# Optimization experiments

Hardware: AMD Instinct MI355X
Metric: run time of the kernel (lower is better)

## Reference

```python
import jax, jax.numpy as jnp
import numpy as np

B, S, D = 2, 2048, 1024
H = 16
DH = D // H  # 64

def setup_inputs() -> dict:
    key = jax.random.key(0)
    k1, k2, k3, k4 = jax.random.split(key, 4)
    scale = 0.02
    x = jax.random.normal(k1, (B, S, D), dtype=jnp.float32)
    W_query = jax.random.normal(k2, (D, D), dtype=jnp.float32) * scale
    W_key = jax.random.normal(k3, (D, D), dtype=jnp.float32) * scale
    W_value = jax.random.normal(k4, (D, D), dtype=jnp.float32) * scale
    return {"x": x, "W_query": W_query, "W_key": W_key, "W_value": W_value}

def reference(x, W_query, W_key, W_value):
    b, n, d_in = x.shape
    # project and split heads: [b, h, n, dh]
    q = (x @ W_query).reshape(b, n, H, DH).transpose(0, 2, 1, 3)
    k = (x @ W_key).reshape(b, n, H, DH).transpose(0, 2, 1, 3)
    v = (x @ W_value).reshape(b, n, H, DH).transpose(0, 2, 1, 3)
    # raw scores, then causal mask (strict upper triangle -> -inf)
    scores = jnp.einsum('bhqd,bhkd->bhqk', q, k)
    causal = jnp.tril(jnp.ones((n, n), dtype=bool))  # True = keep
    scores = jnp.where(causal, scores, -jnp.inf)
    weights = jax.nn.softmax(scores / jnp.sqrt(jnp.float32(DH)), axis=-1)
    ctx = jnp.einsum('bhqk,bhkd->bhqd', weights, v)
    return ctx.transpose(0, 2, 1, 3).reshape(b, n, H * DH)
```

## Files before the change

### kernel.cpp

```cpp
#include <hip/hip_runtime.h>
#include <hip/hip_bf16.h>

#define S_LEN   2048
#define D_MODEL 1024
#define N_HEADS 16
#define D_HEAD  64
#define HEAD_ELEMS (2048ull * 64ull)
#define MAT_ELEMS  (4096ull * 1024ull)
#define W_ELEMS    (1024ull * 1024ull)

typedef __attribute__((ext_vector_type(8))) short short8_t;
typedef __attribute__((ext_vector_type(4))) short short4_t;
typedef __attribute__((ext_vector_type(4))) float f32x4;

__device__ __forceinline__ short f2bf(float f) {
    __hip_bfloat16 h = __float2bfloat16(f);
    union { __hip_bfloat16 h; short s; } cv;
    cv.h = h;
    return cv.s;
}

#define GLD_LDS16(gptr, lptr) \
    __builtin_amdgcn_global_load_lds( \
        (const __attribute__((address_space(1))) unsigned int*)(gptr), \
        (__attribute__((address_space(3))) unsigned int*)(lptr), 16, 0, 0)

__global__ __launch_bounds__(256) void convert_x_kernel(
    const float* __restrict__ x, short* __restrict__ xb)
{
    const int i = (blockIdx.x * 256 + threadIdx.x) * 8;
    const float4 v0 = *(const float4*)(x + i);
    const float4 v1 = *(const float4*)(x + i + 4);
    short8_t u;
    u[0] = f2bf(v0.x); u[1] = f2bf(v0.y); u[2] = f2bf(v0.z); u[3] = f2bf(v0.w);
    u[4] = f2bf(v1.x); u[5] = f2bf(v1.y); u[6] = f2bf(v1.z); u[7] = f2bf(v1.w);
    *(short8_t*)(xb + i) = u;
}

__global__ __launch_bounds__(256) void transpose_w_kernel(
    const float* __restrict__ Wq, const float* __restrict__ Wk,
    const float* __restrict__ Wv, short* __restrict__ wt)
{
    const int k0 = blockIdx.x * 64;
    const int n0 = blockIdx.y * 64;
    const int which = blockIdx.z;
    const float* W = (which == 0) ? Wq : (which == 1) ? Wk : Wv;
    short* out = wt + (size_t)which * W_ELEMS;

    __shared__ float Ts[64][68];
    const int t = threadIdx.x;
    {
        const int c4 = (t & 15) * 4;
#pragma unroll
        for (int i = 0; i < 4; ++i) {
            const int r = (t >> 4) + i * 16;
            const float4 v = *(const float4*)(W + (size_t)(k0 + r) * D_MODEL + n0 + c4);
            Ts[c4 + 0][r] = v.x; Ts[c4 + 1][r] = v.y;
            Ts[c4 + 2][r] = v.z; Ts[c4 + 3][r] = v.w;
        }
    }
    __syncthreads();
    const int nl = t >> 2;
#pragma unroll
    for (int s = 0; s < 2; ++s) {
        const int koff = (t & 3) * 8 + s * 32;
        short8_t u;
#pragma unroll
        for (int j = 0; j < 8; ++j) u[j] = f2bf(Ts[nl][koff + j]);
        *(short8_t*)(out + (size_t)(n0 + nl) * D_MODEL + k0 + koff) = u;
    }
}

__global__ __launch_bounds__(256, 3) void qkv_mfma_gemm_kernel(
    const short* __restrict__ xb,
    const short* __restrict__ wt,
    short* __restrict__ qkv)
{
    const int mBlock = blockIdx.x * 128;
    const int nBlock = blockIdx.y * 128;
    const int which  = blockIdx.z;
    const short* Bt = wt + (size_t)which * W_ELEMS;
    short* outBase  = qkv + (size_t)which * MAT_ELEMS;

    __shared__ short As[128 * 32];
    __shared__ short Bs[128 * 32];

    const int t    = threadIdx.x;
    const int w    = t >> 6;
    const int lane = t & 63;
    const int n16  = lane & 15;
    const int quad = lane >> 4;
    const int mq   = (w & 1) * 64;
    const int nq   = (w >> 1) * 64;

    f32x4 acc[4][4];
#pragma unroll
    for (int i = 0; i < 4; ++i)
#pragma unroll
        for (int j = 0; j < 4; ++j) acc[i][j] = (f32x4){0.f, 0.f, 0.f, 0.f};

    const int off0 = w * 2048 + lane * 16;
    const int off1 = off0 + 1024;
    const int r0s = off0 >> 6, k0s = (off0 & 63) >> 1;
    const int r1s = off1 >> 6, k1s = (off1 & 63) >> 1;
    const short* gA0 = xb + (size_t)(mBlock + r0s) * D_MODEL + k0s;
    const short* gA1 = xb + (size_t)(mBlock + r1s) * D_MODEL + k1s;
    const short* gB0 = Bt + (size_t)(nBlock + r0s) * D_MODEL + k0s;
    const short* gB1 = Bt + (size_t)(nBlock + r1s) * D_MODEL + k1s;
    short* lA0 = As + w * 1024;
    short* lA1 = As + w * 1024 + 512;
    short* lB0 = Bs + w * 1024;
    short* lB1 = Bs + w * 1024 + 512;

    for (int k0 = 0; k0 < D_MODEL; k0 += 32) {
        __syncthreads();
        GLD_LDS16(gA0 + k0, lA0);
        GLD_LDS16(gA1 + k0, lA1);
        GLD_LDS16(gB0 + k0, lB0);
        GLD_LDS16(gB1 + k0, lB1);
        __syncthreads();

        short8_t af[4], bf[4];
#pragma unroll
        for (int mt = 0; mt < 4; ++mt)
            af[mt] = *(const short8_t*)&As[(mq + mt * 16 + n16) * 32 + quad * 8];
#pragma unroll
        for (int nt = 0; nt < 4; ++nt)
            bf[nt] = *(const short8_t*)&Bs[(nq + nt * 16 + n16) * 32 + quad * 8];
#pragma unroll
        for (int mt = 0; mt < 4; ++mt)
#pragma unroll
            for (int nt = 0; nt < 4; ++nt)
                acc[mt][nt] = __builtin_amdgcn_mfma_f32_16x16x32_bf16(
                    af[mt], bf[nt], acc[mt][nt], 0, 0, 0);
    }

    const float oscale = (which == 0) ? 0.125f : 1.0f;
    if (which < 2) {
#pragma unroll
        for (int mt = 0; mt < 4; ++mt) {
#pragma unroll
            for (int nt = 0; nt < 4; ++nt) {
                const int n = nBlock + nq + nt * 16 + n16;
                const int h = n >> 6, dh = n & 63;
#pragma unroll
                for (int reg = 0; reg < 4; ++reg) {
                    const int m = mBlock + mq + mt * 16 + quad * 4 + reg;
                    const int bb = m >> 11, ss = m & 2047;
                    outBase[((size_t)(bb * N_HEADS + h) * S_LEN + ss) * D_HEAD + dh] =
                        f2bf(acc[mt][nt][reg] * oscale);
                }
            }
        }
    } else {
#pragma unroll
        for (int mt = 0; mt < 4; ++mt) {
            const int m0 = mBlock + mq + mt * 16 + quad * 4;
            const int bb = m0 >> 11, ss0 = m0 & 2047;
#pragma unroll
            for (int nt = 0; nt < 4; ++nt) {
                const int n = nBlock + nq + nt * 16 + n16;
                const int h = n >> 6, dh = n & 63;
                short4_t u;
                u[0] = f2bf(acc[mt][nt][0]); u[1] = f2bf(acc[mt][nt][1]);
                u[2] = f2bf(acc[mt][nt][2]); u[3] = f2bf(acc[mt][nt][3]);
                *(short4_t*)(outBase +
                    ((size_t)((bb * N_HEADS + h) * D_HEAD + dh)) * S_LEN + ss0) = u;
            }
        }
    }
}

__global__ __launch_bounds__(256, 2) void attn_mfma_kernel(
    const short* __restrict__ qkv,
    float* __restrict__ out)
{
    const int bh   = blockIdx.x;
    const int pr   = blockIdx.y;
    const int t    = threadIdx.x;
    const int w    = t >> 6;
    const int lane = t & 63;
    const int n    = lane & 15;
    const int quad = lane >> 4;

    const short* Q  = qkv + (size_t)bh * HEAD_ELEMS;
    const short* K  = qkv + MAT_ELEMS + (size_t)bh * HEAD_ELEMS;
    const short* Vt = qkv + 2 * MAT_ELEMS + (size_t)bh * HEAD_ELEMS;

    __shared__ __align__(16) short Ks[64 * 64];
    __shared__ __align__(16) short Vs[64 * 64];
    __shared__ __align__(16) short Ps[4][16][72];

    const int srow0 = w * 16 + (lane >> 3);
    const int srow1 = srow0 + 8;
    const int sd0 = ((lane & 7) ^ (srow0 & 7)) * 8;
    const int sd1 = ((lane & 7) ^ (srow1 & 7)) * 8;
    const short* gK0 = K + srow0 * 64 + sd0;
    const short* gK1 = K + srow1 * 64 + sd1;
    const short* gV0 = Vt + (size_t)srow0 * S_LEN + sd0;
    const short* gV1 = Vt + (size_t)srow1 * S_LEN + sd1;
    short* lK0 = Ks + (w * 16) * 64;
    short* lK1 = Ks + (w * 16 + 8) * 64;
    short* lV0 = Vs + (w * 16) * 64;
    short* lV1 = Vs + (w * 16 + 8) * 64;

    const int pcK = ((quad ^ (n & 7))) * 8;

    const int bb = bh >> 4;
    const int hh = bh & 15;

    for (int pass = 0; pass < 2; ++pass) {
        const int qb = pass ? (31 - pr) : pr;
        const int r0 = qb * 64 + w * 16;
        const int qrow = r0 + n;

        const short8_t bq0 = *(const short8_t*)(Q + (size_t)qrow * D_HEAD + quad * 8);
        const short8_t bq1 = *(const short8_t*)(Q + (size_t)qrow * D_HEAD + quad * 8 + 32);

        float m = -__builtin_inff();
        float l = 0.f;
        f32x4 o[4];
#pragma unroll
        for (int f = 0; f < 4; ++f) o[f] = (f32x4){0.f, 0.f, 0.f, 0.f};

        for (int tile = 0; tile <= qb; ++tile) {
            const int j0 = tile * 64;
            __syncthreads();
            GLD_LDS16(gK0 + j0 * 64, lK0);
            GLD_LDS16(gK1 + j0 * 64, lK1);
            GLD_LDS16(gV0 + j0, lV0);
            GLD_LDS16(gV1 + j0, lV1);
            __syncthreads();

            f32x4 st[4];
#pragma unroll
            for (int kg = 0; kg < 4; ++kg) {
                const int rbase = (kg * 16 + n) * 64;
                const short8_t a0 = *(const short8_t*)&Ks[rbase + pcK];
                const short8_t a1 = *(const short8_t*)&Ks[rbase + (pcK ^ 32)];
                f32x4 acc = (f32x4){0.f, 0.f, 0.f, 0.f};
                acc = __builtin_amdgcn_mfma_f32_16x16x32_bf16(a0, bq0, acc, 0, 0, 0);
                acc = __builtin_amdgcn_mfma_f32_16x16x32_bf16(a1, bq1, acc, 0, 0, 0);
                st[kg] = acc;
            }

            float p[16];
            float mx = -__builtin_inff();
            if (tile == qb) {
#pragma unroll
                for (int kg = 0; kg < 4; ++kg)
#pragma unroll
                    for (int r = 0; r < 4; ++r) {
                        const int key = j0 + kg * 16 + quad * 4 + r;
                        float s = st[kg][r];
                        s = (key <= qrow) ? s : -__builtin_inff();
                        p[kg * 4 + r] = s;
                        mx = fmaxf(mx, s);
                    }
            } else {
#pragma unroll
                for (int i = 0; i < 16; ++i) {
                    const float s = st[i >> 2][i & 3];
                    p[i] = s;
                    mx = fmaxf(mx, s);
                }
            }
            mx = fmaxf(mx, __shfl_xor(mx, 16));
            mx = fmaxf(mx, __shfl_xor(mx, 32));
            const float mnew  = fmaxf(m, mx);
            const float alpha = __expf(m - mnew);
            float ls = 0.f;
#pragma unroll
            for (int i = 0; i < 16; ++i) {
                p[i] = __expf(p[i] - mnew);
                ls += p[i];
            }
            ls += __shfl_xor(ls, 16);
            ls += __shfl_xor(ls, 32);
            l = l * alpha + ls;
            m = mnew;
#pragma unroll
            for (int f = 0; f < 4; ++f) {
                o[f][0] *= alpha; o[f][1] *= alpha; o[f][2] *= alpha; o[f][3] *= alpha;
            }

#pragma unroll
            for (int kg = 0; kg < 4; ++kg) {
                const unsigned int b0 = __builtin_bit_cast(unsigned int, p[kg * 4 + 0]);
                const unsigned int b1 = __builtin_bit_cast(unsigned int, p[kg * 4 + 1]);
                const unsigned int b2 = __builtin_bit_cast(unsigned int, p[kg * 4 + 2]);
                const unsigned int b3 = __builtin_bit_cast(unsigned int, p[kg * 4 + 3]);
                uint2 pk;
                pk.x = (b0 >> 16) | (b1 & 0xffff0000u);
                pk.y = (b2 >> 16) | (b3 & 0xffff0000u);
                *(uint2*)&Ps[w][n][kg * 16 + quad * 4] = pk;
            }
            const short8_t pb0 = *(const short8_t*)&Ps[w][n][quad * 8];
            const short8_t pb1 = *(const short8_t*)&Ps[w][n][quad * 8 + 32];

#pragma unroll
            for (int f = 0; f < 4; ++f) {
                const int rbase = (f * 16 + n) * 64;
                const short8_t va0 = *(const short8_t*)&Vs[rbase + pcK];
                const short8_t va1 = *(const short8_t*)&Vs[rbase + (pcK ^ 32)];
                o[f] = __builtin_amdgcn_mfma_f32_16x16x32_bf16(va0, pb0, o[f], 0, 0, 0);
                o[f] = __builtin_amdgcn_mfma_f32_16x16x32_bf16(va1, pb1, o[f], 0, 0, 0);
            }
        }

        __syncthreads();
        float* Os = (float*)((w < 2) ? Ks : Vs) + (w & 1) * 1024;
        const float inv_l = 1.0f / l;
#pragma unroll
        for (int f = 0; f < 4; ++f) {
            const int c  = f * 4 + quad;
            const int pc = c ^ n;
            f32x4 q4;
            q4[0] = o[f][0] * inv_l; q4[1] = o[f][1] * inv_l;
            q4[2] = o[f][2] * inv_l; q4[3] = o[f][3] * inv_l;
            *(f32x4*)&Os[n * 64 + pc * 4] = q4;
        }
#pragma unroll
        for (int rr = 0; rr < 4; ++rr) {
            const int row = rr * 4 + quad;
            const int pc  = n ^ row;
            const f32x4 val = *(const f32x4*)&Os[row * 64 + pc * 4];
            *(f32x4*)(out + ((size_t)(bb * S_LEN + r0 + row)) * D_MODEL
                          + hh * D_HEAD + n * 4) = val;
        }
    }
}

extern "C" void kernel_launch(void* const* d_in, const int* in_sizes, int n_in,
                              void* d_out, int out_size, void* d_ws, size_t ws_size,
                              hipStream_t stream) {
    const float* x  = (const float*)d_in[0];
    const float* Wq = (const float*)d_in[1];
    const float* Wk = (const float*)d_in[2];
    const float* Wv = (const float*)d_in[3];
    float* out = (float*)d_out;

    short* xb  = (short*)d_ws;
    short* wt  = xb + MAT_ELEMS;
    short* qkv = wt + 3 * W_ELEMS;

    convert_x_kernel<<<dim3(MAT_ELEMS / (256 * 8)), 256, 0, stream>>>(x, xb);
    transpose_w_kernel<<<dim3(16, 16, 3), 256, 0, stream>>>(Wq, Wk, Wv, wt);

    qkv_mfma_gemm_kernel<<<dim3(32, 8, 3), 256, 0, stream>>>(xb, wt, qkv);

    attn_mfma_kernel<<<dim3(2 * N_HEADS, 16), 256, 0, stream>>>(qkv, out);
}
```

Measured before the change: 155.0 us.

## Double-buffer K/V tiles in attention and use exp2 softmax with lazy rescale

The attention kernel now double-buffers the K and V LDS tiles. The next tile's global-to-LDS load is issued before the current tile's MFMAs, so one barrier per tile replaces two. The query projection folds log2(e) into its output scale so the softmax can use the hardware exp2. It also skips the running-max rescale of the output accumulators when the new row max exceeds the old one by at most 8 in log2 units. s_setprio is raised around the MFMA blocks, and LDS use doubles for the K/V buffers in exchange for the load/compute overlap.

Result: no change. 153.7 us (-0.8%).

```diff
diff --git a/kernel.cpp b/kernel.cpp
--- a/kernel.cpp
+++ b/kernel.cpp
@@ -135,7 +135,7 @@
                     af[mt], bf[nt], acc[mt][nt], 0, 0, 0);
     }
 
-    const float oscale = (which == 0) ? 0.125f : 1.0f;
+    const float oscale = (which == 0) ? 0.125f * 1.44269504089f : 1.0f;
     if (which < 2) {
 #pragma unroll
         for (int mt = 0; mt < 4; ++mt) {
@@ -187,8 +187,8 @@
     const short* K  = qkv + MAT_ELEMS + (size_t)bh * HEAD_ELEMS;
     const short* Vt = qkv + 2 * MAT_ELEMS + (size_t)bh * HEAD_ELEMS;
 
-    __shared__ __align__(16) short Ks[64 * 64];
-    __shared__ __align__(16) short Vs[64 * 64];
+    __shared__ __align__(16) short Ks[2][64 * 64];
+    __shared__ __align__(16) short Vs[2][64 * 64];
     __shared__ __align__(16) short Ps[4][16][72];
 
     const int srow0 = w * 16 + (lane >> 3);
@@ -199,10 +199,8 @@
     const short* gK1 = K + srow1 * 64 + sd1;
     const short* gV0 = Vt + (size_t)srow0 * S_LEN + sd0;
     const short* gV1 = Vt + (size_t)srow1 * S_LEN + sd1;
-    short* lK0 = Ks + (w * 16) * 64;
-    short* lK1 = Ks + (w * 16 + 8) * 64;
-    short* lV0 = Vs + (w * 16) * 64;
-    short* lV1 = Vs + (w * 16 + 8) * 64;
+    const int lo0 = (w * 16) * 64;
+    const int lo1 = (w * 16 + 8) * 64;
 
     const int pcK = ((quad ^ (n & 7))) * 8;
 
@@ -223,26 +221,38 @@
 #pragma unroll
         for (int f = 0; f < 4; ++f) o[f] = (f32x4){0.f, 0.f, 0.f, 0.f};
 
+        GLD_LDS16(gK0, &Ks[0][lo0]);
+        GLD_LDS16(gK1, &Ks[0][lo1]);
+        GLD_LDS16(gV0, &Vs[0][lo0]);
+        GLD_LDS16(gV1, &Vs[0][lo1]);
+        __syncthreads();
+
         for (int tile = 0; tile <= qb; ++tile) {
+            const int cur = tile & 1;
+            if (tile < qb) {
+                const int j1 = (tile + 1) * 64;
+                GLD_LDS16(gK0 + j1 * 64, &Ks[cur ^ 1][lo0]);
+                GLD_LDS16(gK1 + j1 * 64, &Ks[cur ^ 1][lo1]);
+                GLD_LDS16(gV0 + j1,      &Vs[cur ^ 1][lo0]);
+                GLD_LDS16(gV1 + j1,      &Vs[cur ^ 1][lo1]);
+            }
             const int j0 = tile * 64;
-            __syncthreads();
-            GLD_LDS16(gK0 + j0 * 64, lK0);
-            GLD_LDS16(gK1 + j0 * 64, lK1);
-            GLD_LDS16(gV0 + j0, lV0);
-            GLD_LDS16(gV1 + j0, lV1);
-            __syncthreads();
+            const short* Kc = Ks[cur];
+            const short* Vc = Vs[cur];
 
             f32x4 st[4];
+            __builtin_amdgcn_s_setprio(1);
 #pragma unroll
             for (int kg = 0; kg < 4; ++kg) {
                 const int rbase = (kg * 16 + n) * 64;
-                const short8_t a0 = *(const short8_t*)&Ks[rbase + pcK];
-                const short8_t a1 = *(const short8_t*)&Ks[rbase + (pcK ^ 32)];
+                const short8_t a0 = *(const short8_t*)&Kc[rbase + pcK];
+                const short8_t a1 = *(const short8_t*)&Kc[rbase + (pcK ^ 32)];
                 f32x4 acc = (f32x4){0.f, 0.f, 0.f, 0.f};
                 acc = __builtin_amdgcn_mfma_f32_16x16x32_bf16(a0, bq0, acc, 0, 0, 0);
                 acc = __builtin_amdgcn_mfma_f32_16x16x32_bf16(a1, bq1, acc, 0, 0, 0);
                 st[kg] = acc;
             }
+            __builtin_amdgcn_s_setprio(0);
 
             float p[16];
             float mx = -__builtin_inff();
@@ -267,21 +277,34 @@
             }
             mx = fmaxf(mx, __shfl_xor(mx, 16));
             mx = fmaxf(mx, __shfl_xor(mx, 32));
-            const float mnew  = fmaxf(m, mx);
-            const float alpha = __expf(m - mnew);
+
             float ls = 0.f;
-#pragma unroll
-            for (int i = 0; i < 16; ++i) {
-                p[i] = __expf(p[i] - mnew);
-                ls += p[i];
-            }
-            ls += __shfl_xor(ls, 16);
-            ls += __shfl_xor(ls, 32);
-            l = l * alpha + ls;
-            m = mnew;
-#pragma unroll
-            for (int f = 0; f < 4; ++f) {
-                o[f][0] *= alpha; o[f][1] *= alpha; o[f][2] *= alpha; o[f][3] *= alpha;
+            if (__all(mx <= m + 8.0f)) {
+#pragma unroll
+                for (int i = 0; i < 16; ++i) {
+                    p[i] = __builtin_amdgcn_exp2f(p[i] - m);
+                    ls += p[i];
+                }
+                ls += __shfl_xor(ls, 16);
+                ls += __shfl_xor(ls, 32);
+                l += ls;
+            } else {
+                const float mnew  = fmaxf(m, mx);
+                const float alpha = __builtin_amdgcn_exp2f(m - mnew);
+#pragma unroll
+                for (int i = 0; i < 16; ++i) {
+                    p[i] = __builtin_amdgcn_exp2f(p[i] - mnew);
+                    ls += p[i];
+                }
+                ls += __shfl_xor(ls, 16);
+                ls += __shfl_xor(ls, 32);
+                l = l * alpha + ls;
+                m = mnew;
+#pragma unroll
+                for (int f = 0; f < 4; ++f) {
+                    o[f][0] *= alpha; o[f][1] *= alpha;
+                    o[f][2] *= alpha; o[f][3] *= alpha;
+                }
             }
 
 #pragma unroll
@@ -298,18 +321,21 @@
             const short8_t pb0 = *(const short8_t*)&Ps[w][n][quad * 8];
             const short8_t pb1 = *(const short8_t*)&Ps[w][n][quad * 8 + 32];
 
+            __builtin_amdgcn_s_setprio(1);
 #pragma unroll
             for (int f = 0; f < 4; ++f) {
                 const int rbase = (f * 16 + n) * 64;
-                const short8_t va0 = *(const short8_t*)&Vs[rbase + pcK];
-                const short8_t va1 = *(const short8_t*)&Vs[rbase + (pcK ^ 32)];
+                const short8_t va0 = *(const short8_t*)&Vc[rbase + pcK];
+                const short8_t va1 = *(const short8_t*)&Vc[rbase + (pcK ^ 32)];
                 o[f] = __builtin_amdgcn_mfma_f32_16x16x32_bf16(va0, pb0, o[f], 0, 0, 0);
                 o[f] = __builtin_amdgcn_mfma_f32_16x16x32_bf16(va1, pb1, o[f], 0, 0, 0);
             }
-        }
-
-        __syncthreads();
-        float* Os = (float*)((w < 2) ? Ks : Vs) + (w & 1) * 1024;
+            __builtin_amdgcn_s_setprio(0);
+
+            __syncthreads();
+        }
+
+        float* Os = (float*)((w < 2) ? (void*)Ks : (void*)Vs) + (w & 1) * 1024;
         const float inv_l = 1.0f / l;
 #pragma unroll
         for (int f = 0; f < 4; ++f) {
@@ -328,6 +354,7 @@
             *(f32x4*)(out + ((size_t)(bb * S_LEN + r0 + row)) * D_MODEL
                           + hh * D_HEAD + n * 4) = val;
         }
+        __syncthreads();
     }
 }
 
```
